# Kernel tuning notes

Measured on AMD Instinct MI355X. Metric: run time of the kernel, lower is better.

The kernel has to match this reference:

```python
import jax, jax.numpy as jnp
import numpy as np

B, IN, OUT, E, H, K = 8192, 1024, 256, 16, 512, 3
EPS = 1e-10


def setup_inputs() -> dict:
    key = jax.random.key(0)
    ks = jax.random.split(key, 5)
    scaled = lambda k, shape, fan: jax.random.normal(k, shape, jnp.float32) / np.sqrt(fan)
    return {
        "x": jax.random.normal(ks[0], (B, IN), jnp.float32),
        # torch init is zeros for w_gate (degenerate ties); use small random for a meaningful reference
        "w_gate": jax.random.normal(ks[1], (IN, E), jnp.float32) * 0.02,
        "W1": scaled(ks[2], (E, IN, H), IN),
        "b1": jnp.zeros((E, H), jnp.float32),
        "W2": scaled(ks[3], (E, H, OUT), H),
        "b2": jnp.zeros((E, OUT), jnp.float32),
    }


def _cv_squared(v):
    # torch .var() is unbiased (ddof=1)
    return jnp.var(v, ddof=1) / (jnp.mean(v) ** 2 + EPS)


def reference(x, w_gate, W1, b1, W2, b2):
    # --- top-k gating (eval mode: clean logits, no noise) ---
    logits = x @ w_gate                                   # [B, E]
    top_vals, top_idx = jax.lax.top_k(logits, K)          # [B, K]
    top_gates = jax.nn.softmax(top_vals, axis=-1)         # softmax over selected k
    rows = jnp.arange(logits.shape[0])[:, None]
    gates = jnp.zeros_like(logits).at[rows, top_idx].set(top_gates)  # sparse gates [B, E]

    # --- load-balancing loss ---
    importance = gates.sum(0)
    load = (gates > 0).sum(0).astype(jnp.float32)         # _gates_to_load (eval path)
    loss = _cv_squared(importance) + _cv_squared(load)

    # --- experts (MLP stand-in; dense compute, sparse combine via zero gates) ---
    h = jax.nn.relu(jnp.einsum('bi,eih->beh', x, W1) + b1)  # [B, E, H]
    expert_out = jnp.einsum('beh,eho->beo', h, W2) + b2     # [B, E, OUT]

    # combine: equivalent to SparseDispatcher gather/split/scatter-add with gate weighting
    y = jnp.einsum('be,beo->bo', gates, expert_out)         # [B, OUT]
    return y, loss
```

## Files before the change

kernel.cpp:

```cpp
#include <hip/hip_runtime.h>

#define B_ 8192
#define IN_ 1024
#define OUT_ 256
#define E_ 16
#define KTOP 3
#define H_ 512
#define MAXSLOTS 26624
#define NTILES 208
#define HBLK 16
#define GBLK 512

typedef __bf16 bf16;
typedef __bf16 bf16x4 __attribute__((ext_vector_type(4)));
typedef __bf16 bf16x8 __attribute__((ext_vector_type(8)));
typedef float f32x4 __attribute__((ext_vector_type(4)));

__device__ __forceinline__ void async16(const bf16* g, bf16* l) {
    __builtin_amdgcn_global_load_lds(
        (const __attribute__((address_space(1))) void*)g,
        (__attribute__((address_space(3))) void*)l,
        16, 0, 0);
}

__global__ __launch_bounds__(256) void k_stage1(
    const float* __restrict__ x, const float* __restrict__ wg,
    const float* __restrict__ W1, const float* __restrict__ W2,
    bf16* __restrict__ xbf, int* __restrict__ top_idx, float* __restrict__ top_gate,
    int* __restrict__ partial,
    bf16* __restrict__ w1t, bf16* __restrict__ w2t,
    int* __restrict__ row_ids, bf16* __restrict__ zero_row, int* __restrict__ tile_expert) {
    __shared__ __align__(16) float smem[16448];
    __shared__ int lcnt[16];
    int bx = blockIdx.x;
    int t = threadIdx.x;
    if (bx < GBLK) {
        float4* swgT4 = (float4*)smem;
        const float4* wg4 = (const float4*)wg;
        if (t < 16) lcnt[t] = 0;
#pragma unroll
        for (int i = 0; i < 16; i++) {
            int p = (t & 3) * 4 + ((t >> 2) & 3);
            int slot = i * 16 + (t >> 4);
            swgT4[p * 257 + slot] = wg4[i * 256 + t];
        }
        __syncthreads();
        int wv = t >> 6, lane = t & 63;
#pragma unroll
        for (int pr = 0; pr < 2; ++pr) {
            int row = bx * 16 + wv * 4 + pr * 2;
            const float4* xra = (const float4*)(x + (size_t)row * IN_);
            const float4* xrb = (const float4*)(x + (size_t)(row + 1) * IN_);
            float4 xa[4], xb4[4];
#pragma unroll
            for (int q = 0; q < 4; q++) { xa[q] = xra[lane + 64 * q]; xb4[q] = xrb[lane + 64 * q]; }
#pragma unroll
            for (int q = 0; q < 4; q++) {
                bf16x4 ca, cb;
                ca[0] = (bf16)xa[q].x; ca[1] = (bf16)xa[q].y; ca[2] = (bf16)xa[q].z; ca[3] = (bf16)xa[q].w;
                cb[0] = (bf16)xb4[q].x; cb[1] = (bf16)xb4[q].y; cb[2] = (bf16)xb4[q].z; cb[3] = (bf16)xb4[q].w;
                *(bf16x4*)(xbf + (size_t)row * IN_ + (size_t)(lane + 64 * q) * 4) = ca;
                *(bf16x4*)(xbf + (size_t)(row + 1) * IN_ + (size_t)(lane + 64 * q) * 4) = cb;
            }
            float acca[16], accb[16];
#pragma unroll
            for (int e = 0; e < 16; e++) { acca[e] = 0.f; accb[e] = 0.f; }
#pragma unroll
            for (int q = 0; q < 4; q++) {
                float sa[4] = {xa[q].x, xa[q].y, xa[q].z, xa[q].w};
                float sb[4] = {xb4[q].x, xb4[q].y, xb4[q].z, xb4[q].w};
#pragma unroll
                for (int jj = 0; jj < 4; jj++) {
#pragma unroll
                    for (int e4 = 0; e4 < 4; e4++) {
                        float4 w4 = swgT4[(e4 * 4 + jj) * 257 + lane + 64 * q];
                        acca[e4 * 4 + 0] += sa[jj] * w4.x;
                        acca[e4 * 4 + 1] += sa[jj] * w4.y;
                        acca[e4 * 4 + 2] += sa[jj] * w4.z;
                        acca[e4 * 4 + 3] += sa[jj] * w4.w;
                        accb[e4 * 4 + 0] += sb[jj] * w4.x;
                        accb[e4 * 4 + 1] += sb[jj] * w4.y;
                        accb[e4 * 4 + 2] += sb[jj] * w4.z;
                        accb[e4 * 4 + 3] += sb[jj] * w4.w;
                    }
                }
            }
#pragma unroll
            for (int e = 0; e < 16; e++) {
#pragma unroll
                for (int s = 32; s > 0; s >>= 1) {
                    acca[e] += __shfl_xor(acca[e], s, 64);
                    accb[e] += __shfl_xor(accb[e], s, 64);
                }
            }
            if (lane < 2) {
                float v[16];
#pragma unroll
                for (int e = 0; e < 16; e++) v[e] = lane ? accb[e] : acca[e];
                int rsel = row + lane;
                int idx[KTOP];
                float val[KTOP];
#pragma unroll
                for (int k = 0; k < KTOP; k++) {
                    int best = 0;
                    float bv = v[0];
                    for (int e = 1; e < 16; e++) {
                        if (v[e] > bv) { bv = v[e]; best = e; }
                    }
                    idx[k] = best; val[k] = bv; v[best] = -1e30f;
                }
                float e1 = __expf(val[1] - val[0]);
                float e2 = __expf(val[2] - val[0]);
                float inv = 1.f / (1.f + e1 + e2);
                float g[KTOP] = {inv, e1 * inv, e2 * inv};
#pragma unroll
                for (int k = 0; k < KTOP; k++) {
                    top_idx[rsel * KTOP + k] = idx[k];
                    top_gate[rsel * KTOP + k] = g[k];
                    atomicAdd(&lcnt[idx[k]], 1);
                }
            }
        }
        __syncthreads();
        if (t < 16) partial[bx * 16 + t] = lcnt[t];
        return;
    }
    if (bx >= 3072) {
        if (bx < 3176) {
            row_ids[(bx - 3072) * 256 + t] = -1;
        } else {
#pragma unroll
            for (int i = 0; i < 4; i++) zero_row[t * 4 + i] = (bf16)0.f;
            if (t < NTILES) tile_expert[t] = -1;
        }
        return;
    }
    float (*tile)[65] = (float(*)[65])smem;
    const float* in; bf16* out; int Kd, Nd, e, tk, tn;
    if (bx < 2560) {
        int b1x = bx - 512;
        in = W1; out = w1t; Kd = IN_; Nd = H_;
        e = b1x >> 7; int tt = b1x & 127; tk = tt >> 3; tn = tt & 7;
    } else {
        int b2x = bx - 2560;
        in = W2; out = w2t; Kd = H_; Nd = OUT_;
        e = b2x >> 5; int tt = b2x & 31; tk = tt >> 2; tn = tt & 3;
    }
    int r = t >> 6, c = t & 63;
    const float* src = in + ((size_t)e * Kd + tk * 64) * Nd + (size_t)tn * 64;
#pragma unroll
    for (int i = 0; i < 16; i++) {
        int rr = r + i * 4;
        tile[rr][c] = src[(size_t)rr * Nd + c];
    }
    __syncthreads();
    bf16* dst = out + ((size_t)e * Nd + tn * 64) * Kd + (size_t)tk * 64;
#pragma unroll
    for (int i = 0; i < 16; i++) {
        int rr = r + i * 4;
        dst[(size_t)rr * Kd + c] = (bf16)tile[c][rr];
    }
}

__global__ __launch_bounds__(256) void k_scatterscan(
    const int* __restrict__ top_idx, const float* __restrict__ top_gate,
    const int* __restrict__ partial,
    int* __restrict__ counts, int* __restrict__ tile_expert,
    int* __restrict__ row_ids, int* __restrict__ rowslot,
    float* __restrict__ partial_imp) {
    __shared__ int segsum[16][16];
    __shared__ int tote[16];
    __shared__ int sbase[16];
    __shared__ int lcnt[16];
    __shared__ float limp[16];
    int t = threadIdx.x;
    int blk = blockIdx.x;
    int e = t & 15, seg = t >> 4;
    int s = 0;
#pragma unroll
    for (int i = 0; i < GBLK / 16; i++) s += partial[(seg * (GBLK / 16) + i) * 16 + e];
    segsum[seg][e] = s;
    if (t < 16) { lcnt[t] = 0; limp[t] = 0.f; }
    __syncthreads();
    if (t < 16) {
        int total = 0, pre = 0;
        for (int sg = 0; sg < 16; sg++) {
            int v = segsum[sg][t];
            total += v;
            if (sg < blk) pre += v;
        }
        tote[t] = total;
        segsum[0][t] = pre;
    }
    __syncthreads();
    if (t < 16) {
        int off = 0;
        for (int ee = 0; ee < 16; ee++) {
            if (ee == t) break;
            off += (tote[ee] + 127) & ~127;
        }
        sbase[t] = off + segsum[0][t];
        if (blk == 0) {
            counts[t] = tote[t];
            int pd = (tote[t] + 127) & ~127;
            for (int tt = off >> 7; tt < (off + pd) >> 7; ++tt) tile_expert[tt] = t;
        }
    }
    __syncthreads();
#pragma unroll
    for (int j = 0; j < 6; j++) {
        int gid = blk * 1536 + j * 256 + t;
        int ee = top_idx[gid];
        float g = top_gate[gid];
        int rank = atomicAdd(&lcnt[ee], 1);
        atomicAdd(&limp[ee], g);
        int slot = sbase[ee] + rank;
        row_ids[slot] = gid / KTOP;
        rowslot[gid] = slot;
    }
    __syncthreads();
    if (t < 16) partial_imp[blk * 16 + t] = limp[t];
}

#define VWAIT(N) asm volatile("s_waitcnt vmcnt(" #N ")" ::: "memory")
__global__ __launch_bounds__(512) void k_fused(
    const bf16* __restrict__ xbf, const bf16* __restrict__ w1t,
    const float* __restrict__ b1, const bf16* __restrict__ w2t,
    const float* __restrict__ b2, const int* __restrict__ row_ids,
    const int* __restrict__ tile_expert, const bf16* __restrict__ zero_row,
    bf16* __restrict__ eout) {
    int e = tile_expert[blockIdx.x];
    if (e < 0) return;
    int slot_base = blockIdx.x * 128;
    __shared__ __align__(16) bf16 smem[69632];
    bf16* hs = smem;
    bf16* pb0 = smem + 32768;
    bf16* pb1 = smem + 32768 + 12288;
    bf16* pb2 = smem + 32768 + 24576;
    int t = threadIdx.x;
    int cg = (t & 3) ^ ((t >> 3) & 3);
    int rid = row_ids[slot_base + (t >> 2)];
    const bf16* gA = ((rid >= 0) ? xbf + (size_t)rid * IN_ : zero_row) + cg * 8;
    const bf16* gB1[2];
    const bf16* gB2[2];
#pragma unroll
    for (int j = 0; j < 2; j++) {
        int m = j * 128 + (t >> 2);
        gB1[j] = w1t + ((size_t)e * H_ + m) * IN_ + cg * 8;
        gB2[j] = w2t + ((size_t)e * OUT_ + m) * H_ + cg * 8;
    }
    int w = t >> 6, lane = t & 63;
    int wm = (w & 1) * 64, wn = (w >> 1) * 64;
    int lm = lane & 15, lq = lane >> 4;
    int aidx[4], bidx[4], hrow[4], hx[4];
#pragma unroll
    for (int i = 0; i < 4; i++) {
        int ra = wm + i * 16 + lm;
        int rb = wn + i * 16 + lm;
        aidx[i] = ra * 4 + (lq ^ ((ra >> 1) & 3));
        bidx[i] = rb * 4 + (lq ^ ((rb >> 1) & 3));
        hrow[i] = ra * 32;
        hx[i] = ra & 7;
    }
    float rbias1[2][4], rbias2[4];
#pragma unroll
    for (int c2 = 0; c2 < 2; ++c2)
#pragma unroll
        for (int ni = 0; ni < 4; ++ni) rbias1[c2][ni] = b1[e * H_ + c2 * 256 + wn + ni * 16 + lm];
#pragma unroll
    for (int ni = 0; ni < 4; ++ni) rbias2[ni] = b2[e * OUT_ + wn + ni * 16 + lm];
#pragma unroll
    for (int c2 = 0; c2 < 2; ++c2)
#pragma unroll
        for (int ni = 0; ni < 4; ++ni) asm volatile("" : "+v"(rbias1[c2][ni]));
#pragma unroll
    for (int ni = 0; ni < 4; ++ni) asm volatile("" : "+v"(rbias2[ni]));

    auto stageG1 = [&](bf16* buf, int c, int k) {
        async16(gA + k * 32, buf + t * 8);
        async16(gB1[0] + (size_t)c * (256 * IN_) + k * 32, buf + 4096 + t * 8);
        async16(gB1[1] + (size_t)c * (256 * IN_) + k * 32, buf + 4096 + (512 + t) * 8);
    };
    auto stageG2 = [&](bf16* buf, int c, int s) {
        const bf16* p0 = gB2[0] + c * 256 + s * 32;
        async16(p0, buf + t * 8);
        async16(gB2[1] + c * 256 + s * 32, buf + (512 + t) * 8);
        async16(p0, buf + t * 8);
    };

    f32x4 acc2[4][4] = {};
    bf16 *bufA = pb0, *bufB = pb1, *bufC = pb2;
    stageG1(bufA, 0, 0);
    stageG1(bufB, 0, 1);
#pragma unroll
    for (int c = 0; c < 2; ++c) {
        f32x4 acc1[4][4] = {};
        for (int k = 0; k < 32; ++k) {
            VWAIT(3);
            __builtin_amdgcn_s_barrier();
            __builtin_amdgcn_sched_barrier(0);
            const bf16x8* Av = (const bf16x8*)bufA;
            const bf16x8* Bv = (const bf16x8*)(bufA + 4096);
            bf16x8 af[4], bfv[4];
#pragma unroll
            for (int i = 0; i < 4; i++) af[i] = Av[aidx[i]];
#pragma unroll
            for (int i = 0; i < 4; i++) bfv[i] = Bv[bidx[i]];
#pragma unroll
            for (int mi = 0; mi < 4; mi++)
#pragma unroll
                for (int ni = 0; ni < 4; ni++)
                    acc1[mi][ni] = __builtin_amdgcn_mfma_f32_16x16x32_bf16(af[mi], bfv[ni], acc1[mi][ni], 0, 0, 0);
            if (k < 30) stageG1(bufC, c, k + 2);
            else        stageG2(bufC, c, k - 30);
            bf16* tmpb = bufA; bufA = bufB; bufB = bufC; bufC = tmpb;
        }
#pragma unroll
        for (int mi = 0; mi < 4; mi++) {
#pragma unroll
            for (int ni = 0; ni < 4; ni++) {
                int col = wn + ni * 16 + lm;
                float bias = rbias1[c][ni];
#pragma unroll
                for (int r = 0; r < 4; r++) {
                    int row = wm + mi * 16 + lq * 4 + r;
                    float v = acc1[mi][ni][r] + bias;
                    v = v > 0.f ? v : 0.f;
                    hs[row * 256 + (((col >> 3) ^ (row & 7)) << 3) + (col & 7)] = (bf16)v;
                }
            }
        }
        asm volatile("s_waitcnt lgkmcnt(0)" ::: "memory");
#pragma unroll
        for (int s = 0; s < 8; ++s) {
            if (c == 1 && s == 7) { VWAIT(0); } else { VWAIT(3); }
            __builtin_amdgcn_s_barrier();
            __builtin_amdgcn_sched_barrier(0);
            const bf16x8* Hv = (const bf16x8*)hs;
            const bf16x8* B2v = (const bf16x8*)bufA;
            bf16x8 af[4], bfv[4];
#pragma unroll
            for (int i = 0; i < 4; i++) af[i] = Hv[hrow[i] + ((s * 4 + lq) ^ hx[i])];
#pragma unroll
            for (int i = 0; i < 4; i++) bfv[i] = B2v[bidx[i]];
#pragma unroll
            for (int mi = 0; mi < 4; mi++)
#pragma unroll
                for (int ni = 0; ni < 4; ni++)
                    acc2[mi][ni] = __builtin_amdgcn_mfma_f32_16x16x32_bf16(af[mi], bfv[ni], acc2[mi][ni], 0, 0, 0);
            if (s < 6)       stageG2(bufC, c, s + 2);
            else if (c == 0) stageG1(bufC, 1, s - 6);
            bf16* tmpb = bufA; bufA = bufB; bufB = bufC; bufC = tmpb;
        }
    }
#pragma unroll
    for (int mi = 0; mi < 4; mi++) {
#pragma unroll
        for (int ni = 0; ni < 4; ni++) {
            int colg = wn + ni * 16 + lm;
            float bias = rbias2[ni];
#pragma unroll
            for (int r = 0; r < 4; r++) {
                int rowl = wm + mi * 16 + lq * 4 + r;
                eout[(size_t)(slot_base + rowl) * OUT_ + colg] = (bf16)(acc2[mi][ni][r] + bias);
            }
        }
    }
}

__global__ __launch_bounds__(256) void k_combine(
    const bf16* __restrict__ eout, const int* __restrict__ rowslot,
    const float* __restrict__ top_gate, float* __restrict__ y,
    const float* __restrict__ partial_imp, const int* __restrict__ counts,
    float* __restrict__ loss_out) {
    int t = threadIdx.x;
    if (blockIdx.x == B_ / 4) {
        __shared__ float imp[16];
        if (t < 16) {
            float s = 0.f;
#pragma unroll
            for (int b = 0; b < HBLK; b++) s += partial_imp[b * 16 + t];
            imp[t] = s;
        }
        __syncthreads();
        if (t == 0) {
            float si = 0.f, sl = 0.f;
            for (int e = 0; e < E_; e++) { si += imp[e]; sl += (float)counts[e]; }
            float mi_ = si / (float)E_, ml_ = sl / (float)E_;
            float vi = 0.f, vl = 0.f;
            for (int e = 0; e < E_; e++) {
                float d = imp[e] - mi_; vi += d * d;
                float d2 = (float)counts[e] - ml_; vl += d2 * d2;
            }
            vi /= (float)(E_ - 1); vl /= (float)(E_ - 1);
            *loss_out = vi / (mi_ * mi_ + 1e-10f) + vl / (ml_ * ml_ + 1e-10f);
        }
        return;
    }
    int b = blockIdx.x * 4 + (t >> 6);
    int lane = t & 63;
    int s0 = rowslot[b * 3], s1 = rowslot[b * 3 + 1], s2 = rowslot[b * 3 + 2];
    float g0 = top_gate[b * 3], g1 = top_gate[b * 3 + 1], g2 = top_gate[b * 3 + 2];
    bf16x4 v0 = *(const bf16x4*)(eout + (size_t)s0 * OUT_ + lane * 4);
    bf16x4 v1 = *(const bf16x4*)(eout + (size_t)s1 * OUT_ + lane * 4);
    bf16x4 v2 = *(const bf16x4*)(eout + (size_t)s2 * OUT_ + lane * 4);
    float4 r;
    r.x = g0 * (float)v0[0] + g1 * (float)v1[0] + g2 * (float)v2[0];
    r.y = g0 * (float)v0[1] + g1 * (float)v1[1] + g2 * (float)v2[1];
    r.z = g0 * (float)v0[2] + g1 * (float)v1[2] + g2 * (float)v2[2];
    r.w = g0 * (float)v0[3] + g1 * (float)v1[3] + g2 * (float)v2[3];
    ((float4*)y)[(size_t)b * 64 + lane] = r;
}

extern "C" void kernel_launch(void* const* d_in, const int* in_sizes, int n_in,
                              void* d_out, int out_size, void* d_ws, size_t ws_size,
                              hipStream_t stream) {
    (void)in_sizes; (void)n_in; (void)out_size; (void)ws_size;
    const float* x = (const float*)d_in[0];
    const float* wgate = (const float*)d_in[1];
    const float* W1 = (const float*)d_in[2];
    const float* b1 = (const float*)d_in[3];
    const float* W2 = (const float*)d_in[4];
    const float* b2 = (const float*)d_in[5];
    float* y = (float*)d_out;

    char* p = (char*)d_ws;
    auto alloc = [&](size_t bytes) {
        char* q = p;
        p += (bytes + 255) & ~(size_t)255;
        return q;
    };
    bf16* xbf = (bf16*)alloc((size_t)B_ * IN_ * 2);
    bf16* w1t = (bf16*)alloc((size_t)E_ * H_ * IN_ * 2);
    bf16* w2t = (bf16*)alloc((size_t)E_ * OUT_ * H_ * 2);
    bf16* eout = (bf16*)alloc((size_t)MAXSLOTS * OUT_ * 2);
    int* row_ids = (int*)alloc((size_t)MAXSLOTS * 4);
    int* rowslot = (int*)alloc((size_t)B_ * KTOP * 4);
    int* top_idx = (int*)alloc((size_t)B_ * KTOP * 4);
    float* top_gate = (float*)alloc((size_t)B_ * KTOP * 4);
    int* counts = (int*)alloc(E_ * 4);
    int* partial = (int*)alloc((size_t)GBLK * E_ * 4);
    float* partial_imp = (float*)alloc(HBLK * E_ * 4);
    int* tile_expert = (int*)alloc(NTILES * 4);
    bf16* zero_row = (bf16*)alloc(IN_ * 2);

    k_stage1<<<dim3(3177), dim3(256), 0, stream>>>(
        x, wgate, W1, W2, xbf, top_idx, top_gate, partial, w1t, w2t,
        row_ids, zero_row, tile_expert);
    k_scatterscan<<<dim3(HBLK), dim3(256), 0, stream>>>(
        top_idx, top_gate, partial, counts, tile_expert, row_ids, rowslot, partial_imp);
    k_fused<<<dim3(NTILES), dim3(512), 0, stream>>>(
        xbf, w1t, b1, w2t, b2, row_ids, tile_expert, zero_row, eout);
    k_combine<<<dim3(B_ / 4 + 1), dim3(256), 0, stream>>>(
        eout, rowslot, top_gate, y, partial_imp, counts, y + (size_t)B_ * OUT_);
}
```

Measured before the change: 186.3 us.

## Load GEMM operands directly from global into registers instead of LDS staging

Replaces the triple-buffered async global-to-LDS staging of the x and weight tiles with direct per-lane global loads into registers, double-buffered across k steps. LDS is cut to only the hidden-activation buffer, and launch bounds ask for two blocks per CU to raise occupancy. The risk is redundant global traffic, since each operand row is reloaded by several waves with no LDS sharing, plus higher register pressure from the double-buffered fragments.

```diff
diff --git a/kernel.cpp b/kernel.cpp
--- a/kernel.cpp
+++ b/kernel.cpp
@@ -15,13 +15,6 @@
 typedef __bf16 bf16x4 __attribute__((ext_vector_type(4)));
 typedef __bf16 bf16x8 __attribute__((ext_vector_type(8)));
 typedef float f32x4 __attribute__((ext_vector_type(4)));
-
-__device__ __forceinline__ void async16(const bf16* g, bf16* l) {
-    __builtin_amdgcn_global_load_lds(
-        (const __attribute__((address_space(1))) void*)g,
-        (__attribute__((address_space(3))) void*)l,
-        16, 0, 0);
-}
 
 __global__ __launch_bounds__(256) void k_stage1(
     const float* __restrict__ x, const float* __restrict__ wg,
@@ -222,8 +215,7 @@
     if (t < 16) partial_imp[blk * 16 + t] = limp[t];
 }
 
-#define VWAIT(N) asm volatile("s_waitcnt vmcnt(" #N ")" ::: "memory")
-__global__ __launch_bounds__(512) void k_fused(
+__global__ __launch_bounds__(512, 2) void k_fused(
     const bf16* __restrict__ xbf, const bf16* __restrict__ w1t,
     const float* __restrict__ b1, const bf16* __restrict__ w2t,
     const float* __restrict__ b2, const int* __restrict__ row_ids,
@@ -232,95 +224,68 @@
     int e = tile_expert[blockIdx.x];
     if (e < 0) return;
     int slot_base = blockIdx.x * 128;
-    __shared__ __align__(16) bf16 smem[69632];
-    bf16* hs = smem;
-    bf16* pb0 = smem + 32768;
-    bf16* pb1 = smem + 32768 + 12288;
-    bf16* pb2 = smem + 32768 + 24576;
+    __shared__ __align__(16) bf16 hs[32768];
     int t = threadIdx.x;
-    int cg = (t & 3) ^ ((t >> 3) & 3);
-    int rid = row_ids[slot_base + (t >> 2)];
-    const bf16* gA = ((rid >= 0) ? xbf + (size_t)rid * IN_ : zero_row) + cg * 8;
-    const bf16* gB1[2];
-    const bf16* gB2[2];
-#pragma unroll
-    for (int j = 0; j < 2; j++) {
-        int m = j * 128 + (t >> 2);
-        gB1[j] = w1t + ((size_t)e * H_ + m) * IN_ + cg * 8;
-        gB2[j] = w2t + ((size_t)e * OUT_ + m) * H_ + cg * 8;
-    }
     int w = t >> 6, lane = t & 63;
     int wm = (w & 1) * 64, wn = (w >> 1) * 64;
     int lm = lane & 15, lq = lane >> 4;
-    int aidx[4], bidx[4], hrow[4], hx[4];
+    const bf16* pa[4];
+    const bf16* pb1[4];
+    const bf16* pb2[4];
+    int hrow[4], hx[4];
 #pragma unroll
     for (int i = 0; i < 4; i++) {
         int ra = wm + i * 16 + lm;
         int rb = wn + i * 16 + lm;
-        aidx[i] = ra * 4 + (lq ^ ((ra >> 1) & 3));
-        bidx[i] = rb * 4 + (lq ^ ((rb >> 1) & 3));
+        int rid = row_ids[slot_base + ra];
+        pa[i] = ((rid >= 0) ? xbf + (size_t)rid * IN_ : zero_row) + lq * 8;
+        pb1[i] = w1t + ((size_t)e * H_ + rb) * IN_ + lq * 8;
+        pb2[i] = w2t + ((size_t)e * OUT_ + rb) * H_ + lq * 8;
         hrow[i] = ra * 32;
         hx[i] = ra & 7;
     }
-    float rbias1[2][4], rbias2[4];
-#pragma unroll
-    for (int c2 = 0; c2 < 2; ++c2)
-#pragma unroll
-        for (int ni = 0; ni < 4; ++ni) rbias1[c2][ni] = b1[e * H_ + c2 * 256 + wn + ni * 16 + lm];
+    float rbias2[4];
 #pragma unroll
     for (int ni = 0; ni < 4; ++ni) rbias2[ni] = b2[e * OUT_ + wn + ni * 16 + lm];
-#pragma unroll
-    for (int c2 = 0; c2 < 2; ++c2)
-#pragma unroll
-        for (int ni = 0; ni < 4; ++ni) asm volatile("" : "+v"(rbias1[c2][ni]));
-#pragma unroll
-    for (int ni = 0; ni < 4; ++ni) asm volatile("" : "+v"(rbias2[ni]));
-
-    auto stageG1 = [&](bf16* buf, int c, int k) {
-        async16(gA + k * 32, buf + t * 8);
-        async16(gB1[0] + (size_t)c * (256 * IN_) + k * 32, buf + 4096 + t * 8);
-        async16(gB1[1] + (size_t)c * (256 * IN_) + k * 32, buf + 4096 + (512 + t) * 8);
-    };
-    auto stageG2 = [&](bf16* buf, int c, int s) {
-        const bf16* p0 = gB2[0] + c * 256 + s * 32;
-        async16(p0, buf + t * 8);
-        async16(gB2[1] + c * 256 + s * 32, buf + (512 + t) * 8);
-        async16(p0, buf + t * 8);
-    };
 
     f32x4 acc2[4][4] = {};
-    bf16 *bufA = pb0, *bufB = pb1, *bufC = pb2;
-    stageG1(bufA, 0, 0);
-    stageG1(bufB, 0, 1);
-#pragma unroll
+#pragma unroll 1
     for (int c = 0; c < 2; ++c) {
+        size_t boff = (size_t)c * (256 * IN_);
+        float rbias1[4];
+#pragma unroll
+        for (int ni = 0; ni < 4; ++ni) rbias1[ni] = b1[e * H_ + c * 256 + wn + ni * 16 + lm];
         f32x4 acc1[4][4] = {};
+        bf16x8 fa[2][4], fb[2][4];
+#pragma unroll
+        for (int i = 0; i < 4; i++) {
+            fa[0][i] = *(const bf16x8*)(pa[i]);
+            fb[0][i] = *(const bf16x8*)(pb1[i] + boff);
+        }
+#pragma unroll
         for (int k = 0; k < 32; ++k) {
-            VWAIT(3);
-            __builtin_amdgcn_s_barrier();
-            __builtin_amdgcn_sched_barrier(0);
-            const bf16x8* Av = (const bf16x8*)bufA;
-            const bf16x8* Bv = (const bf16x8*)(bufA + 4096);
-            bf16x8 af[4], bfv[4];
-#pragma unroll
-            for (int i = 0; i < 4; i++) af[i] = Av[aidx[i]];
-#pragma unroll
-            for (int i = 0; i < 4; i++) bfv[i] = Bv[bidx[i]];
+            int p = k & 1;
+            if (k < 31) {
+                int off = (k + 1) * 32;
+#pragma unroll
+                for (int i = 0; i < 4; i++) {
+                    fa[p ^ 1][i] = *(const bf16x8*)(pa[i] + off);
+                    fb[p ^ 1][i] = *(const bf16x8*)(pb1[i] + boff + off);
+                }
+            }
 #pragma unroll
             for (int mi = 0; mi < 4; mi++)
 #pragma unroll
                 for (int ni = 0; ni < 4; ni++)
-                    acc1[mi][ni] = __builtin_amdgcn_mfma_f32_16x16x32_bf16(af[mi], bfv[ni], acc1[mi][ni], 0, 0, 0);
-            if (k < 30) stageG1(bufC, c, k + 2);
-            else        stageG2(bufC, c, k - 30);
-            bf16* tmpb = bufA; bufA = bufB; bufB = bufC; bufC = tmpb;
-        }
+                    acc1[mi][ni] = __builtin_amdgcn_mfma_f32_16x16x32_bf16(fa[p][mi], fb[p][ni], acc1[mi][ni], 0, 0, 0);
+        }
+        __syncthreads();
 #pragma unroll
         for (int mi = 0; mi < 4; mi++) {
 #pragma unroll
             for (int ni = 0; ni < 4; ni++) {
                 int col = wn + ni * 16 + lm;
-                float bias = rbias1[c][ni];
+                float bias = rbias1[ni];
 #pragma unroll
                 for (int r = 0; r < 4; r++) {
                     int row = wm + mi * 16 + lq * 4 + r;
@@ -330,27 +295,29 @@
                 }
             }
         }
-        asm volatile("s_waitcnt lgkmcnt(0)" ::: "memory");
+        __syncthreads();
+        const bf16x8* Hv = (const bf16x8*)hs;
+        bf16x8 ha[2][4], wb[2][4];
+#pragma unroll
+        for (int i = 0; i < 4; i++) {
+            ha[0][i] = Hv[hrow[i] + (lq ^ hx[i])];
+            wb[0][i] = *(const bf16x8*)(pb2[i] + c * 256);
+        }
 #pragma unroll
         for (int s = 0; s < 8; ++s) {
-            if (c == 1 && s == 7) { VWAIT(0); } else { VWAIT(3); }
-            __builtin_amdgcn_s_barrier();
-            __builtin_amdgcn_sched_barrier(0);
-            const bf16x8* Hv = (const bf16x8*)hs;
-            const bf16x8* B2v = (const bf16x8*)bufA;
-            bf16x8 af[4], bfv[4];
-#pragma unroll
-            for (int i = 0; i < 4; i++) af[i] = Hv[hrow[i] + ((s * 4 + lq) ^ hx[i])];
-#pragma unroll
-            for (int i = 0; i < 4; i++) bfv[i] = B2v[bidx[i]];
+            int p = s & 1;
+            if (s < 7) {
+#pragma unroll
+                for (int i = 0; i < 4; i++) {
+                    ha[p ^ 1][i] = Hv[hrow[i] + (((s + 1) * 4 + lq) ^ hx[i])];
+                    wb[p ^ 1][i] = *(const bf16x8*)(pb2[i] + c * 256 + (s + 1) * 32);
+                }
+            }
 #pragma unroll
             for (int mi = 0; mi < 4; mi++)
 #pragma unroll
                 for (int ni = 0; ni < 4; ni++)
-                    acc2[mi][ni] = __builtin_amdgcn_mfma_f32_16x16x32_bf16(af[mi], bfv[ni], acc2[mi][ni], 0, 0, 0);
-            if (s < 6)       stageG2(bufC, c, s + 2);
-            else if (c == 0) stageG1(bufC, 1, s - 6);
-            bf16* tmpb = bufA; bufA = bufB; bufB = bufC; bufC = tmpb;
+                    acc2[mi][ni] = __builtin_amdgcn_mfma_f32_16x16x32_bf16(ha[p][mi], wb[p][ni], acc2[mi][ni], 0, 0, 0);
         }
     }
 #pragma unroll
```

New measurement: 401.8 us. 2.16x slower.

## Load expert A operand directly into registers, shrink LDS and target two blocks per CU

Applied to the files above, without the earlier changes.

The fused expert MLP kernel stops staging the gathered x rows through LDS and instead loads each wave's A fragments straight from global memory into registers, one k-step ahead in a software pipeline. The B staging buffers shrink accordingly, and a redundant duplicate async copy in the W2 stage is removed. Total LDS drops and launch bounds request 2 blocks per CU so occupancy can rise. In exchange, every wave redundantly fetches its x rows from global memory or L2, and register pressure rises under the tighter launch bound.

```diff
diff --git a/kernel.cpp b/kernel.cpp
--- a/kernel.cpp
+++ b/kernel.cpp
@@ -223,7 +223,34 @@
 }
 
 #define VWAIT(N) asm volatile("s_waitcnt vmcnt(" #N ")" ::: "memory")
-__global__ __launch_bounds__(512) void k_fused(
+#define BARR do { __builtin_amdgcn_s_barrier(); __builtin_amdgcn_sched_barrier(0); } while (0)
+#define ROT do { bf16* _tmp = bA; bA = bB; bB = bC; bC = _tmp; } while (0)
+#define LOADA(DST, K) do { \
+    _Pragma("unroll") for (int _i = 0; _i < 4; _i++) \
+        DST[_i] = *(const bf16x8*)(pa[_i] + (K) * 32); \
+    __builtin_amdgcn_sched_barrier(0); \
+} while (0)
+#define G1STEP(BUF, FA) do { \
+    const bf16x8* _Bv = (const bf16x8*)(BUF); \
+    bf16x8 _bfv[4]; \
+    _Pragma("unroll") for (int _i = 0; _i < 4; _i++) _bfv[_i] = _Bv[bidx[_i]]; \
+    _Pragma("unroll") for (int _mi = 0; _mi < 4; _mi++) \
+        _Pragma("unroll") for (int _ni = 0; _ni < 4; _ni++) \
+            acc1[_mi][_ni] = __builtin_amdgcn_mfma_f32_16x16x32_bf16(FA[_mi], _bfv[_ni], acc1[_mi][_ni], 0, 0, 0); \
+} while (0)
+#define G2STEP(BUF, S) do { \
+    const bf16x8* _Hv = (const bf16x8*)hs; \
+    const bf16x8* _B2v = (const bf16x8*)(BUF); \
+    bf16x8 _ha[4], _bfv[4]; \
+    _Pragma("unroll") for (int _i = 0; _i < 4; _i++) { \
+        _ha[_i] = _Hv[hrow[_i] + (((S) * 4 + lq) ^ hx[_i])]; \
+        _bfv[_i] = _B2v[bidx[_i]]; \
+    } \
+    _Pragma("unroll") for (int _mi = 0; _mi < 4; _mi++) \
+        _Pragma("unroll") for (int _ni = 0; _ni < 4; _ni++) \
+            acc2[_mi][_ni] = __builtin_amdgcn_mfma_f32_16x16x32_bf16(_ha[_mi], _bfv[_ni], acc2[_mi][_ni], 0, 0, 0); \
+} while (0)
+__global__ __launch_bounds__(512, 2) void k_fused(
     const bf16* __restrict__ xbf, const bf16* __restrict__ w1t,
     const float* __restrict__ b1, const bf16* __restrict__ w2t,
     const float* __restrict__ b2, const int* __restrict__ row_ids,
@@ -232,15 +259,13 @@
     int e = tile_expert[blockIdx.x];
     if (e < 0) return;
     int slot_base = blockIdx.x * 128;
-    __shared__ __align__(16) bf16 smem[69632];
+    __shared__ __align__(16) bf16 smem[57344];
     bf16* hs = smem;
-    bf16* pb0 = smem + 32768;
-    bf16* pb1 = smem + 32768 + 12288;
-    bf16* pb2 = smem + 32768 + 24576;
+    bf16* bA = smem + 32768;
+    bf16* bB = smem + 32768 + 8192;
+    bf16* bC = smem + 32768 + 16384;
     int t = threadIdx.x;
     int cg = (t & 3) ^ ((t >> 3) & 3);
-    int rid = row_ids[slot_base + (t >> 2)];
-    const bf16* gA = ((rid >= 0) ? xbf + (size_t)rid * IN_ : zero_row) + cg * 8;
     const bf16* gB1[2];
     const bf16* gB2[2];
 #pragma unroll
@@ -252,12 +277,14 @@
     int w = t >> 6, lane = t & 63;
     int wm = (w & 1) * 64, wn = (w >> 1) * 64;
     int lm = lane & 15, lq = lane >> 4;
-    int aidx[4], bidx[4], hrow[4], hx[4];
+    const bf16* pa[4];
+    int bidx[4], hrow[4], hx[4];
 #pragma unroll
     for (int i = 0; i < 4; i++) {
         int ra = wm + i * 16 + lm;
         int rb = wn + i * 16 + lm;
-        aidx[i] = ra * 4 + (lq ^ ((ra >> 1) & 3));
+        int rid = row_ids[slot_base + ra];
+        pa[i] = ((rid >= 0) ? xbf + (size_t)rid * IN_ : zero_row) + lq * 8;
         bidx[i] = rb * 4 + (lq ^ ((rb >> 1) & 3));
         hrow[i] = ra * 32;
         hx[i] = ra & 7;
@@ -276,45 +303,44 @@
 #pragma unroll
     for (int ni = 0; ni < 4; ++ni) asm volatile("" : "+v"(rbias2[ni]));
 
-    auto stageG1 = [&](bf16* buf, int c, int k) {
-        async16(gA + k * 32, buf + t * 8);
-        async16(gB1[0] + (size_t)c * (256 * IN_) + k * 32, buf + 4096 + t * 8);
-        async16(gB1[1] + (size_t)c * (256 * IN_) + k * 32, buf + 4096 + (512 + t) * 8);
+    auto stageB1 = [&](bf16* buf, int c, int k) {
+        async16(gB1[0] + (size_t)c * (256 * IN_) + k * 32, buf + t * 8);
+        async16(gB1[1] + (size_t)c * (256 * IN_) + k * 32, buf + (512 + t) * 8);
     };
-    auto stageG2 = [&](bf16* buf, int c, int s) {
-        const bf16* p0 = gB2[0] + c * 256 + s * 32;
-        async16(p0, buf + t * 8);
+    auto stageB2 = [&](bf16* buf, int c, int s) {
+        async16(gB2[0] + c * 256 + s * 32, buf + t * 8);
         async16(gB2[1] + c * 256 + s * 32, buf + (512 + t) * 8);
-        async16(p0, buf + t * 8);
     };
 
     f32x4 acc2[4][4] = {};
-    bf16 *bufA = pb0, *bufB = pb1, *bufC = pb2;
-    stageG1(bufA, 0, 0);
-    stageG1(bufB, 0, 1);
+    bf16x8 fa0[4], fa1[4];
+    stageB1(bA, 0, 0);
+    LOADA(fa0, 0);
+    stageB1(bB, 0, 1);
 #pragma unroll
     for (int c = 0; c < 2; ++c) {
         f32x4 acc1[4][4] = {};
-        for (int k = 0; k < 32; ++k) {
-            VWAIT(3);
-            __builtin_amdgcn_s_barrier();
-            __builtin_amdgcn_sched_barrier(0);
-            const bf16x8* Av = (const bf16x8*)bufA;
-            const bf16x8* Bv = (const bf16x8*)(bufA + 4096);
-            bf16x8 af[4], bfv[4];
-#pragma unroll
-            for (int i = 0; i < 4; i++) af[i] = Av[aidx[i]];
-#pragma unroll
-            for (int i = 0; i < 4; i++) bfv[i] = Bv[bidx[i]];
-#pragma unroll
-            for (int mi = 0; mi < 4; mi++)
-#pragma unroll
-                for (int ni = 0; ni < 4; ni++)
-                    acc1[mi][ni] = __builtin_amdgcn_mfma_f32_16x16x32_bf16(af[mi], bfv[ni], acc1[mi][ni], 0, 0, 0);
-            if (k < 30) stageG1(bufC, c, k + 2);
-            else        stageG2(bufC, c, k - 30);
-            bf16* tmpb = bufA; bufA = bufB; bufB = bufC; bufC = tmpb;
-        }
+        for (int kk = 0; kk < 30; kk += 2) {
+            VWAIT(2); BARR;
+            G1STEP(bA, fa0);
+            LOADA(fa1, kk + 1);
+            stageB1(bC, c, kk + 2);
+            ROT;
+            VWAIT(2); BARR;
+            G1STEP(bA, fa1);
+            LOADA(fa0, kk + 2);
+            stageB1(bC, c, kk + 3);
+            ROT;
+        }
+        VWAIT(2); BARR;
+        G1STEP(bA, fa0);
+        LOADA(fa1, 31);
+        stageB2(bC, c, 0);
+        ROT;
+        VWAIT(2); BARR;
+        G1STEP(bA, fa1);
+        stageB2(bC, c, 1);
+        ROT;
 #pragma unroll
         for (int mi = 0; mi < 4; mi++) {
 #pragma unroll
@@ -331,27 +357,24 @@
             }
         }
         asm volatile("s_waitcnt lgkmcnt(0)" ::: "memory");
-#pragma unroll
-        for (int s = 0; s < 8; ++s) {
-            if (c == 1 && s == 7) { VWAIT(0); } else { VWAIT(3); }
-            __builtin_amdgcn_s_barrier();
-            __builtin_amdgcn_sched_barrier(0);
-            const bf16x8* Hv = (const bf16x8*)hs;
-            const bf16x8* B2v = (const bf16x8*)bufA;
-            bf16x8 af[4], bfv[4];
-#pragma unroll
-            for (int i = 0; i < 4; i++) af[i] = Hv[hrow[i] + ((s * 4 + lq) ^ hx[i])];
-#pragma unroll
-            for (int i = 0; i < 4; i++) bfv[i] = B2v[bidx[i]];
-#pragma unroll
-            for (int mi = 0; mi < 4; mi++)
-#pragma unroll
-                for (int ni = 0; ni < 4; ni++)
-                    acc2[mi][ni] = __builtin_amdgcn_mfma_f32_16x16x32_bf16(af[mi], bfv[ni], acc2[mi][ni], 0, 0, 0);
-            if (s < 6)       stageG2(bufC, c, s + 2);
-            else if (c == 0) stageG1(bufC, 1, s - 6);
-            bf16* tmpb = bufA; bufA = bufB; bufB = bufC; bufC = tmpb;
-        }
+        for (int s = 0; s < 6; ++s) {
+            VWAIT(2); BARR;
+            G2STEP(bA, s);
+            stageB2(bC, c, s + 2);
+            ROT;
+        }
+        VWAIT(2); BARR;
+        G2STEP(bA, 6);
+        if (c == 0) {
+            LOADA(fa0, 0);
+            stageB1(bC, 1, 0);
+        }
+        ROT;
+        if (c == 0) { VWAIT(6); } else { VWAIT(0); }
+        BARR;
+        G2STEP(bA, 7);
+        if (c == 0) stageB1(bC, 1, 1);
+        ROT;
     }
 #pragma unroll
     for (int mi = 0; mi < 4; mi++) {
```

Result: slower. 233.8 us (+25.5%).
